# Kernel tuning notes

Hardware: AMD Instinct MI355X
Metric: run time of the kernel (lower is better)

## Reference

```python
import jax, jax.numpy as jnp
import numpy as np

UNITS = 128
ATT_UNITS = 64
NUM_HEADS = 8


def setup_inputs() -> dict:
    key = jax.random.key(0)
    ks = jax.random.split(key, 8)
    N, F, E = 50000, 128, 800000
    x = jax.random.normal(ks[0], (N, F), dtype=jnp.float32)
    edge_index = jax.random.randint(ks[1], (2, E), 0, N, dtype=jnp.int32)
    glorot = lambda k, shp: jax.random.uniform(k, shp, jnp.float32,
                                               -jnp.sqrt(6.0 / (shp[0] + shp[1])),
                                               jnp.sqrt(6.0 / (shp[0] + shp[1])))
    return {
        "x": x,
        "edge_index": edge_index,
        "query_kernel": glorot(ks[2], (F, ATT_UNITS)),
        "query_bias": jnp.zeros((ATT_UNITS,), jnp.float32),
        "key_kernel": glorot(ks[3], (F, ATT_UNITS)),
        "key_bias": jnp.zeros((ATT_UNITS,), jnp.float32),
        "kernel": glorot(ks[4], (F, UNITS)),
        "bias": jnp.zeros((UNITS,), jnp.float32),
    }


def reference(x, edge_index, query_kernel, query_bias, key_kernel, key_bias, kernel, bias):
    N = x.shape[0]
    H = NUM_HEADS
    # add self-loop edges (tf_geometric add_self_loop_edge)
    loop = jnp.arange(N, dtype=edge_index.dtype)
    row = jnp.concatenate([edge_index[0], loop])  # target nodes
    col = jnp.concatenate([edge_index[1], loop])  # source nodes
    E = row.shape[0]

    Q = jax.nn.relu(x @ query_kernel + query_bias)[row]  # [E, A]
    K = jax.nn.relu(x @ key_kernel + key_bias)[col]      # [E, A]
    V = (x @ kernel)[col]                                # [E, U]

    # split feature dim into contiguous head chunks (matches tf.split)
    Qh = Q.reshape(E, H, -1)
    Kh = K.reshape(E, H, -1)
    Vh = V.reshape(E, H, -1)

    score = jnp.sum(Qh * Kh, axis=-1)  # [E, H]
    # segment softmax over edges grouped by target node (row)
    smax = jax.ops.segment_max(score, row, num_segments=N)  # [N, H]
    ex = jnp.exp(score - smax[row])
    ssum = jax.ops.segment_sum(ex, row, num_segments=N)     # [N, H]
    alpha = ex / ssum[row]                                  # [E, H]

    agg = jax.ops.segment_sum(Vh * alpha[..., None], row, num_segments=N)  # [N, H, U/H]
    h = agg.reshape(N, -1) + bias
    return h
```

## Files before the change

### kernel.cpp

```cpp
#include <hip/hip_runtime.h>

#define SHIFT 10.0f
#define CAP 64
#define NXCD 8
#define BSH 7
#define CAPB 3072

typedef __attribute__((ext_vector_type(8))) short bf16x8;
typedef __attribute__((ext_vector_type(4))) float f32x4;
typedef _Float16 half2v __attribute__((ext_vector_type(2)));

__device__ inline uint16_t bf16r(float f) {
    uint32_t u = __float_as_uint(f);
    return (uint16_t)((u + 0x7FFFu + ((u >> 16) & 1u)) >> 16);
}
__device__ inline float bf2f(uint16_t h) {
    return __uint_as_float(((uint32_t)h) << 16);
}
__device__ inline uint32_t pack_bf16x2(float lo, float hi) {
    return (uint32_t)bf16r(lo) | ((uint32_t)bf16r(hi) << 16);
}
__device__ inline uint32_t pack_f16x2(float lo, float hi) {
    uint16_t a = __builtin_bit_cast(uint16_t, (_Float16)lo);
    uint16_t b = __builtin_bit_cast(uint16_t, (_Float16)hi);
    return (uint32_t)a | ((uint32_t)b << 16);
}
__device__ inline half2v as_h2(uint32_t u) {
    return __builtin_bit_cast(half2v, u);
}

#define ABSZ 512
#define AEPT 8
#define PREP_BLKS 32
__global__ __launch_bounds__(ABSZ) void prep_bin(
    const float* __restrict__ Wq, const float* __restrict__ Wk,
    const float* __restrict__ Wv, uint32_t* __restrict__ Wh32,
    uint32_t* __restrict__ Wl32,
    const int* __restrict__ row, const int* __restrict__ col,
    int* __restrict__ bucketCursor, uint32_t* __restrict__ inter, int E)
{
    if (blockIdx.x < PREP_BLKS) {
        int t = blockIdx.x * ABSZ + threadIdx.x;
        int c = t >> 6;
        int k2 = t & 63;
        float f0, f1;
        if (c < 64)       { f0 = Wq[(2 * k2) * 64 + c];          f1 = Wq[(2 * k2 + 1) * 64 + c]; }
        else if (c < 128) { f0 = Wk[(2 * k2) * 64 + (c - 64)];   f1 = Wk[(2 * k2 + 1) * 64 + (c - 64)]; }
        else              { f0 = Wv[(2 * k2) * 128 + (c - 128)]; f1 = Wv[(2 * k2 + 1) * 128 + (c - 128)]; }
        uint16_t h0 = bf16r(f0), h1 = bf16r(f1);
        uint16_t l0 = bf16r(f0 - bf2f(h0)), l1 = bf16r(f1 - bf2f(h1));
        Wh32[t] = (uint32_t)h0 | ((uint32_t)h1 << 16);
        Wl32[t] = (uint32_t)l0 | ((uint32_t)l1 << 16);
        return;
    }

    __shared__ int hist[512];
    __shared__ int basebuf[512];
    const int t = threadIdx.x;
    hist[t] = 0;
    __syncthreads();

    const int base0 = (blockIdx.x - PREP_BLKS) * ABSZ * AEPT;
    uint32_t pk[AEPT];
    int dg[AEPT], rk[AEPT];
#pragma unroll
    for (int k = 0; k < AEPT; ++k) {
        int e = base0 + k * ABSZ + t;
        if (e < E) {
            int r = row[e];
            int c = col[e];
            pk[k] = ((uint32_t)r << 16) | (uint32_t)c;
            dg[k] = r >> BSH;
            rk[k] = atomicAdd(&hist[dg[k]], 1);
        } else dg[k] = -1;
    }
    __syncthreads();

    {
        int h = hist[t];
        basebuf[t] = h ? atomicAdd(&bucketCursor[t], h) : 0;
    }
    __syncthreads();

#pragma unroll
    for (int k = 0; k < AEPT; ++k) {
        if (dg[k] >= 0) {
            int idx = basebuf[dg[k]] + rk[k];
            if (idx < CAPB)
                inter[(size_t)dg[k] * CAPB + idx] = pk[k];
        }
    }
}

__global__ __launch_bounds__(256) void fused_nlb(
    const uint32_t* __restrict__ inter, const int* __restrict__ bucketCursor,
    uint16_t* __restrict__ csr, int* __restrict__ deg,
    const float* __restrict__ x,
    const uint16_t* __restrict__ Wh, const uint16_t* __restrict__ Wl,
    const float* __restrict__ bq, const float* __restrict__ bk,
    uint32_t* __restrict__ Qh, uint32_t* __restrict__ Kh, uint32_t* __restrict__ Vh,
    int N, int NB)
{
    __shared__ uint16_t Ah[64][136];
    __shared__ uint16_t Al[64][136];
    __shared__ int cnt[128];

    if (blockIdx.x < NB) {
        const int b = blockIdx.x;
        const int t = threadIdx.x;
        if (t < 128) cnt[t] = 0;
        __syncthreads();

        const int count = min(bucketCursor[b], CAPB);
        const uint32_t* src = inter + (size_t)b * CAPB;
        for (int i = t; i < count; i += 256) {
            uint32_t u = src[i];
            int r = (int)(u >> 16);
            int pos = atomicAdd(&cnt[r & 127], 1);
            if (pos < CAP - 1)
                csr[(size_t)r * CAP + pos] = (uint16_t)(u & 0xFFFFu);
        }
        __syncthreads();

        const int node = (b << BSH) + t;
        if (t < 128 && node < N) deg[node] = min(cnt[t], CAP - 1);
        return;
    }

    const int tid = threadIdx.x;
    const int lane = tid & 63;
    const int wv = tid >> 6;
    const int block0 = (blockIdx.x - NB) * 64;
    if (block0 >= N) return;

    float4 v[8];
#pragma unroll
    for (int i = 0; i < 8; ++i) {
        int idx = tid + i * 256;
        int node = idx >> 5;
        int c4 = idx & 31;
        v[i] = make_float4(0.f, 0.f, 0.f, 0.f);
        if (block0 + node < N)
            v[i] = reinterpret_cast<const float4*>(x + (size_t)(block0 + node) * 128)[c4];
    }
#pragma unroll
    for (int i = 0; i < 8; ++i) {
        int idx = tid + i * 256;
        int node = idx >> 5;
        int c4 = idx & 31;
        uint16_t hx = bf16r(v[i].x), hy = bf16r(v[i].y), hz = bf16r(v[i].z), hw = bf16r(v[i].w);
        uint2 uh, ul;
        uh.x = (uint32_t)hx | ((uint32_t)hy << 16);
        uh.y = (uint32_t)hz | ((uint32_t)hw << 16);
        ul.x = (uint32_t)bf16r(v[i].x - bf2f(hx)) | ((uint32_t)bf16r(v[i].y - bf2f(hy)) << 16);
        ul.y = (uint32_t)bf16r(v[i].z - bf2f(hz)) | ((uint32_t)bf16r(v[i].w - bf2f(hw)) << 16);
        *reinterpret_cast<uint2*>(&Ah[node][c4 * 4]) = uh;
        *reinterpret_cast<uint2*>(&Al[node][c4 * 4]) = ul;
    }
    __syncthreads();

    f32x4 acc[4][4] = {};
#pragma unroll
    for (int ks = 0; ks < 4; ++ks) {
        bf16x8 bh[4], bl[4];
#pragma unroll
        for (int cf = 0; cf < 4; ++cf) {
            size_t off = (size_t)(wv * 64 + cf * 16 + (lane & 15)) * 128
                         + ks * 32 + (lane >> 4) * 8;
            bh[cf] = *reinterpret_cast<const bf16x8*>(Wh + off);
            bl[cf] = *reinterpret_cast<const bf16x8*>(Wl + off);
        }
#pragma unroll
        for (int rf = 0; rf < 4; ++rf) {
            bf16x8 ah = *reinterpret_cast<const bf16x8*>(
                &Ah[rf * 16 + (lane & 15)][ks * 32 + (lane >> 4) * 8]);
            bf16x8 al = *reinterpret_cast<const bf16x8*>(
                &Al[rf * 16 + (lane & 15)][ks * 32 + (lane >> 4) * 8]);
#pragma unroll
            for (int cf = 0; cf < 4; ++cf)
                acc[rf][cf] = __builtin_amdgcn_mfma_f32_16x16x32_bf16(
                    ah, bh[cf], acc[rf][cf], 0, 0, 0);
#pragma unroll
            for (int cf = 0; cf < 4; ++cf)
                acc[rf][cf] = __builtin_amdgcn_mfma_f32_16x16x32_bf16(
                    ah, bl[cf], acc[rf][cf], 0, 0, 0);
#pragma unroll
            for (int cf = 0; cf < 4; ++cf)
                acc[rf][cf] = __builtin_amdgcn_mfma_f32_16x16x32_bf16(
                    al, bh[cf], acc[rf][cf], 0, 0, 0);
        }
    }

#pragma unroll
    for (int rf = 0; rf < 4; ++rf) {
#pragma unroll
        for (int cf = 0; cf < 4; ++cf) {
            const int ocol = wv * 64 + cf * 16 + (lane & 15);
#pragma unroll
            for (int r = 0; r < 4; ++r) {
                const int orow = rf * 16 + (lane >> 4) * 4 + r;
                const int node = block0 + orow;
                float v2 = acc[rf][cf][r];
                if (wv == 0) {
                    v2 = fmaxf(v2 + bq[ocol], 0.f);
                    float vp = __shfl_xor(v2, 1);
                    if (node < N && !(lane & 1))
                        Qh[(size_t)node * 32 + (ocol >> 1)] = pack_f16x2(v2, vp);
                } else if (wv == 1) {
                    const int ck = ocol - 64;
                    v2 = fmaxf(v2 + bk[ck], 0.f);
                    float vp = __shfl_xor(v2, 1);
                    if (node < N && !(lane & 1))
                        Kh[(size_t)node * 32 + (ck >> 1)] = pack_f16x2(v2, vp);
                } else {
                    const int cv = ocol - 128;
                    float vp = __shfl_xor(v2, 1);
                    if (node < N && !(lane & 1))
                        Vh[(size_t)node * 64 + (cv >> 1)] = pack_bf16x2(v2, vp);
                }
            }
        }
    }
}

__global__ __launch_bounds__(256) void agg6(
    const int* __restrict__ deg_, const uint16_t* __restrict__ csr,
    const uint32_t* __restrict__ Qh, const uint32_t* __restrict__ Kh,
    const uint32_t* __restrict__ Vh, const float* __restrict__ bias,
    float* __restrict__ out, int N)
{
    __shared__ uint32_t qs[4][32];
    __shared__ float es[4][8][36];
    __shared__ int   cis[4][32];

    const int wv = threadIdx.x >> 6;
    const int lane = threadIdx.x & 63;

    const int xcd = blockIdx.x & (NXCD - 1);
    const int nslice = (N + NXCD - 1) / NXCD;
    const int ln = (blockIdx.x >> 3) * 4 + wv;
    if (ln >= nslice) return;
    const int n = xcd * nslice + ln;
    if (n >= N) return;

    const int deg = min(deg_[n], CAP - 1);
    const int tot = deg + 1;

    if (lane < 32) qs[wv][lane] = Qh[(size_t)n * 32 + lane];
    __builtin_amdgcn_wave_barrier();

    const int e2 = lane >> 1;
    const int half = lane & 1;
    const int hrow = lane >> 3;
    const float* esrow = &es[wv][hrow][0];
    const char* Kb = (const char*)Kh;
    const char* Vb = (const char*)Vh;
    const int lane4 = lane << 2;

    float accx = 0.f, accy = 0.f, accL = 0.f;

    for (int base = 0; base < tot; base += 32) {
        const int nn = min(32, tot - base);
        const int idxe = base + e2;
        const bool valide = (idxe < tot);
        int c = n;
        if (valide && idxe < deg) c = (int)csr[(size_t)n * CAP + idxe];
        if (!valide) c = 0;
        cis[wv][e2] = c << 8;

        const uint32_t koff = ((uint32_t)c << 7) + ((uint32_t)half << 6);
        const uint32_t* q16 = &qs[wv][half * 16];
#pragma unroll
        for (int hh = 0; hh < 4; ++hh) {
            uint4 kv = *reinterpret_cast<const uint4*>(Kb + koff + hh * 16);
            const uint32_t* q4 = q16 + hh * 4;
            float s = 0.f;
            s = __builtin_amdgcn_fdot2(as_h2(kv.x), as_h2(q4[0]), s, false);
            s = __builtin_amdgcn_fdot2(as_h2(kv.y), as_h2(q4[1]), s, false);
            s = __builtin_amdgcn_fdot2(as_h2(kv.z), as_h2(q4[2]), s, false);
            s = __builtin_amdgcn_fdot2(as_h2(kv.w), as_h2(q4[3]), s, false);
            es[wv][half * 4 + hh][e2] = valide ? __expf(s - SHIFT) : 0.f;
        }
        __builtin_amdgcn_wave_barrier();

        const int nn4 = (nn + 3) & ~3;
        for (int i = 0; i < nn4; i += 4) {
            int4 c4 = *reinterpret_cast<const int4*>(&cis[wv][i]);
            float4 e4 = *reinterpret_cast<const float4*>(&esrow[i]);
            uint32_t u0 = *reinterpret_cast<const uint32_t*>(Vb + (uint32_t)(c4.x + lane4));
            uint32_t u1 = *reinterpret_cast<const uint32_t*>(Vb + (uint32_t)(c4.y + lane4));
            uint32_t u2 = *reinterpret_cast<const uint32_t*>(Vb + (uint32_t)(c4.z + lane4));
            uint32_t u3 = *reinterpret_cast<const uint32_t*>(Vb + (uint32_t)(c4.w + lane4));
            accx += e4.x * __uint_as_float(u0 << 16);
            accy += e4.x * __uint_as_float(u0 & 0xFFFF0000u);
            accL += e4.x;
            accx += e4.y * __uint_as_float(u1 << 16);
            accy += e4.y * __uint_as_float(u1 & 0xFFFF0000u);
            accL += e4.y;
            accx += e4.z * __uint_as_float(u2 << 16);
            accy += e4.z * __uint_as_float(u2 & 0xFFFF0000u);
            accL += e4.z;
            accx += e4.w * __uint_as_float(u3 << 16);
            accy += e4.w * __uint_as_float(u3 & 0xFFFF0000u);
            accL += e4.w;
        }
        __builtin_amdgcn_wave_barrier();
    }

    float2 b = reinterpret_cast<const float2*>(bias)[lane];
    float inv = 1.0f / accL;
    float2 o;
    o.x = accx * inv + b.x;
    o.y = accy * inv + b.y;
    reinterpret_cast<float2*>(out)[(size_t)n * 64 + lane] = o;
}

extern "C" void kernel_launch(void* const* d_in, const int* in_sizes, int n_in,
                              void* d_out, int out_size, void* d_ws, size_t ws_size,
                              hipStream_t stream) {
    const float* x    = (const float*)d_in[0];
    const int*   ei   = (const int*)d_in[1];
    const float* Wq   = (const float*)d_in[2];
    const float* bq   = (const float*)d_in[3];
    const float* Wk   = (const float*)d_in[4];
    const float* bk   = (const float*)d_in[5];
    const float* Wv   = (const float*)d_in[6];
    const float* bias = (const float*)d_in[7];
    float* out = (float*)d_out;

    const int N = in_sizes[0] / 128;
    const int E = in_sizes[1] / 2;
    const int* row = ei;
    const int* col = ei + E;
    const int NB = (N + (1 << BSH) - 1) >> BSH;

    uint32_t* Qh     = (uint32_t*)d_ws;
    uint32_t* Kh     = Qh + (size_t)N * 32;
    uint32_t* Vh     = Kh + (size_t)N * 32;
    uint32_t* Wh32   = Vh + (size_t)N * 64;
    uint32_t* Wl32   = Wh32 + 16384;
    int*      deg    = (int*)(Wl32 + 16384);
    int*      bcur   = deg + N;
    uint32_t* inter  = (uint32_t*)(bcur + 512);
    uint16_t* csr    = (uint16_t*)(inter + (size_t)NB * CAPB);

    const int nslice = (N + NXCD - 1) / NXCD;
    const int agg_grid = ((nslice + 3) / 4) * NXCD;
    const int nl_grid = (N + 63) / 64;
    const int binA_grid = (E + ABSZ * AEPT - 1) / (ABSZ * AEPT);

    hipMemsetAsync(bcur, 0, 512 * sizeof(int), stream);
    prep_bin<<<PREP_BLKS + binA_grid, ABSZ, 0, stream>>>(
        Wq, Wk, Wv, Wh32, Wl32, row, col, bcur, inter, E);
    fused_nlb<<<NB + nl_grid, 256, 0, stream>>>(
        inter, bcur, csr, deg,
        x, (const uint16_t*)Wh32, (const uint16_t*)Wl32, bq, bk,
        Qh, Kh, Vh, N, NB);
    agg6<<<agg_grid, 256, 0, stream>>>(
        deg, csr, Qh, Kh, Vh, bias, out, N);
}
```

Before: 117.0 us.

## Restructure kernel pipeline: overlap edge binning with projection GEMM, split CSR build

Launches a small weight-prep kernel that also clears the bucket cursors, which replaces the memset. Edge binning phase A now runs in the same grid as the Q/K/V projection GEMM, and CSR finalisation moves into its own kernel. This overlaps the edge scan with the dense work. Q is now stored as fp32 and packed to f16 inside the aggregation kernel, which removes the shuffle in the GEMM epilogue but doubles Q traffic. The change adds one kernel launch, and the binning blocks now use 256 threads with 16 edges each.

```diff
diff --git a/kernel.cpp b/kernel.cpp
--- a/kernel.cpp
+++ b/kernel.cpp
@@ -29,108 +29,85 @@
     return __builtin_bit_cast(half2v, u);
 }
 
-#define ABSZ 512
-#define AEPT 8
-#define PREP_BLKS 32
-__global__ __launch_bounds__(ABSZ) void prep_bin(
+__global__ __launch_bounds__(256) void prep_w(
     const float* __restrict__ Wq, const float* __restrict__ Wk,
     const float* __restrict__ Wv, uint32_t* __restrict__ Wh32,
-    uint32_t* __restrict__ Wl32,
+    uint32_t* __restrict__ Wl32, int* __restrict__ bucketCursor)
+{
+    int t = blockIdx.x * 256 + threadIdx.x;
+    if (t < 512) bucketCursor[t] = 0;
+    if (t >= 256 * 64) return;
+    int c = t >> 6;
+    int k2 = t & 63;
+    float f0, f1;
+    if (c < 64)       { f0 = Wq[(2 * k2) * 64 + c];          f1 = Wq[(2 * k2 + 1) * 64 + c]; }
+    else if (c < 128) { f0 = Wk[(2 * k2) * 64 + (c - 64)];   f1 = Wk[(2 * k2 + 1) * 64 + (c - 64)]; }
+    else              { f0 = Wv[(2 * k2) * 128 + (c - 128)]; f1 = Wv[(2 * k2 + 1) * 128 + (c - 128)]; }
+    uint16_t h0 = bf16r(f0), h1 = bf16r(f1);
+    uint16_t l0 = bf16r(f0 - bf2f(h0)), l1 = bf16r(f1 - bf2f(h1));
+    Wh32[t] = (uint32_t)h0 | ((uint32_t)h1 << 16);
+    Wl32[t] = (uint32_t)l0 | ((uint32_t)l1 << 16);
+}
+
+#define AEPT 16
+__global__ __launch_bounds__(256) void nl_bin(
     const int* __restrict__ row, const int* __restrict__ col,
-    int* __restrict__ bucketCursor, uint32_t* __restrict__ inter, int E)
-{
-    if (blockIdx.x < PREP_BLKS) {
-        int t = blockIdx.x * ABSZ + threadIdx.x;
-        int c = t >> 6;
-        int k2 = t & 63;
-        float f0, f1;
-        if (c < 64)       { f0 = Wq[(2 * k2) * 64 + c];          f1 = Wq[(2 * k2 + 1) * 64 + c]; }
-        else if (c < 128) { f0 = Wk[(2 * k2) * 64 + (c - 64)];   f1 = Wk[(2 * k2 + 1) * 64 + (c - 64)]; }
-        else              { f0 = Wv[(2 * k2) * 128 + (c - 128)]; f1 = Wv[(2 * k2 + 1) * 128 + (c - 128)]; }
-        uint16_t h0 = bf16r(f0), h1 = bf16r(f1);
-        uint16_t l0 = bf16r(f0 - bf2f(h0)), l1 = bf16r(f1 - bf2f(h1));
-        Wh32[t] = (uint32_t)h0 | ((uint32_t)h1 << 16);
-        Wl32[t] = (uint32_t)l0 | ((uint32_t)l1 << 16);
-        return;
-    }
-
-    __shared__ int hist[512];
-    __shared__ int basebuf[512];
-    const int t = threadIdx.x;
-    hist[t] = 0;
-    __syncthreads();
-
-    const int base0 = (blockIdx.x - PREP_BLKS) * ABSZ * AEPT;
-    uint32_t pk[AEPT];
-    int dg[AEPT], rk[AEPT];
-#pragma unroll
-    for (int k = 0; k < AEPT; ++k) {
-        int e = base0 + k * ABSZ + t;
-        if (e < E) {
-            int r = row[e];
-            int c = col[e];
-            pk[k] = ((uint32_t)r << 16) | (uint32_t)c;
-            dg[k] = r >> BSH;
-            rk[k] = atomicAdd(&hist[dg[k]], 1);
-        } else dg[k] = -1;
-    }
-    __syncthreads();
-
-    {
-        int h = hist[t];
-        basebuf[t] = h ? atomicAdd(&bucketCursor[t], h) : 0;
-    }
-    __syncthreads();
-
-#pragma unroll
-    for (int k = 0; k < AEPT; ++k) {
-        if (dg[k] >= 0) {
-            int idx = basebuf[dg[k]] + rk[k];
-            if (idx < CAPB)
-                inter[(size_t)dg[k] * CAPB + idx] = pk[k];
-        }
-    }
-}
-
-__global__ __launch_bounds__(256) void fused_nlb(
-    const uint32_t* __restrict__ inter, const int* __restrict__ bucketCursor,
-    uint16_t* __restrict__ csr, int* __restrict__ deg,
+    int* __restrict__ bucketCursor, uint32_t* __restrict__ inter, int E,
     const float* __restrict__ x,
     const uint16_t* __restrict__ Wh, const uint16_t* __restrict__ Wl,
     const float* __restrict__ bq, const float* __restrict__ bk,
-    uint32_t* __restrict__ Qh, uint32_t* __restrict__ Kh, uint32_t* __restrict__ Vh,
-    int N, int NB)
+    float* __restrict__ Qn, uint32_t* __restrict__ Kh, uint32_t* __restrict__ Vh,
+    int N, int NLG)
 {
     __shared__ uint16_t Ah[64][136];
     __shared__ uint16_t Al[64][136];
-    __shared__ int cnt[128];
-
-    if (blockIdx.x < NB) {
-        const int b = blockIdx.x;
+    __shared__ int hist[512];
+    __shared__ int basebuf[512];
+
+    if (blockIdx.x >= NLG) {
         const int t = threadIdx.x;
-        if (t < 128) cnt[t] = 0;
+        hist[t] = 0; hist[t + 256] = 0;
         __syncthreads();
 
-        const int count = min(bucketCursor[b], CAPB);
-        const uint32_t* src = inter + (size_t)b * CAPB;
-        for (int i = t; i < count; i += 256) {
-            uint32_t u = src[i];
-            int r = (int)(u >> 16);
-            int pos = atomicAdd(&cnt[r & 127], 1);
-            if (pos < CAP - 1)
-                csr[(size_t)r * CAP + pos] = (uint16_t)(u & 0xFFFFu);
+        const int base0 = (blockIdx.x - NLG) * 256 * AEPT;
+        uint32_t pk[AEPT];
+        int dg[AEPT], rk[AEPT];
+#pragma unroll
+        for (int k = 0; k < AEPT; ++k) {
+            int e = base0 + k * 256 + t;
+            if (e < E) {
+                int r = row[e];
+                int c = col[e];
+                pk[k] = ((uint32_t)r << 16) | (uint32_t)c;
+                dg[k] = r >> BSH;
+                rk[k] = atomicAdd(&hist[dg[k]], 1);
+            } else dg[k] = -1;
         }
         __syncthreads();
 
-        const int node = (b << BSH) + t;
-        if (t < 128 && node < N) deg[node] = min(cnt[t], CAP - 1);
+#pragma unroll
+        for (int b2 = 0; b2 < 2; ++b2) {
+            int i = t + b2 * 256;
+            int h = hist[i];
+            basebuf[i] = h ? atomicAdd(&bucketCursor[i], h) : 0;
+        }
+        __syncthreads();
+
+#pragma unroll
+        for (int k = 0; k < AEPT; ++k) {
+            if (dg[k] >= 0) {
+                int idx = basebuf[dg[k]] + rk[k];
+                if (idx < CAPB)
+                    inter[(size_t)dg[k] * CAPB + idx] = pk[k];
+            }
+        }
         return;
     }
 
     const int tid = threadIdx.x;
     const int lane = tid & 63;
     const int wv = tid >> 6;
-    const int block0 = (blockIdx.x - NB) * 64;
+    const int block0 = blockIdx.x * 64;
     if (block0 >= N) return;
 
     float4 v[8];
@@ -203,9 +180,7 @@
                 float v2 = acc[rf][cf][r];
                 if (wv == 0) {
                     v2 = fmaxf(v2 + bq[ocol], 0.f);
-                    float vp = __shfl_xor(v2, 1);
-                    if (node < N && !(lane & 1))
-                        Qh[(size_t)node * 32 + (ocol >> 1)] = pack_f16x2(v2, vp);
+                    if (node < N) Qn[(size_t)node * 64 + ocol] = v2;
                 } else if (wv == 1) {
                     const int ck = ocol - 64;
                     v2 = fmaxf(v2 + bk[ck], 0.f);
@@ -223,9 +198,34 @@
     }
 }
 
+__global__ __launch_bounds__(256) void bin_b(
+    const uint32_t* __restrict__ inter, const int* __restrict__ bucketCursor,
+    uint16_t* __restrict__ csr, int* __restrict__ deg, int N)
+{
+    __shared__ int cnt[128];
+    const int b = blockIdx.x;
+    const int t = threadIdx.x;
+    if (t < 128) cnt[t] = 0;
+    __syncthreads();
+
+    const int count = min(bucketCursor[b], CAPB);
+    const uint32_t* src = inter + (size_t)b * CAPB;
+    for (int i = t; i < count; i += 256) {
+        uint32_t u = src[i];
+        int r = (int)(u >> 16);
+        int pos = atomicAdd(&cnt[r & 127], 1);
+        if (pos < CAP - 1)
+            csr[(size_t)r * CAP + pos] = (uint16_t)(u & 0xFFFFu);
+    }
+    __syncthreads();
+
+    const int node = (b << BSH) + t;
+    if (t < 128 && node < N) deg[node] = min(cnt[t], CAP - 1);
+}
+
 __global__ __launch_bounds__(256) void agg6(
     const int* __restrict__ deg_, const uint16_t* __restrict__ csr,
-    const uint32_t* __restrict__ Qh, const uint32_t* __restrict__ Kh,
+    const float* __restrict__ Qn, const uint32_t* __restrict__ Kh,
     const uint32_t* __restrict__ Vh, const float* __restrict__ bias,
     float* __restrict__ out, int N)
 {
@@ -246,7 +246,10 @@
     const int deg = min(deg_[n], CAP - 1);
     const int tot = deg + 1;
 
-    if (lane < 32) qs[wv][lane] = Qh[(size_t)n * 32 + lane];
+    if (lane < 32) {
+        float2 qq = reinterpret_cast<const float2*>(Qn + (size_t)n * 64)[lane];
+        qs[wv][lane] = pack_f16x2(qq.x, qq.y);
+    }
     __builtin_amdgcn_wave_barrier();
 
     const int e2 = lane >> 1;
@@ -334,8 +337,8 @@
     const int* col = ei + E;
     const int NB = (N + (1 << BSH) - 1) >> BSH;
 
-    uint32_t* Qh     = (uint32_t*)d_ws;
-    uint32_t* Kh     = Qh + (size_t)N * 32;
+    float*    Qn     = (float*)d_ws;
+    uint32_t* Kh     = (uint32_t*)(Qn + (size_t)N * 64);
     uint32_t* Vh     = Kh + (size_t)N * 32;
     uint32_t* Wh32   = Vh + (size_t)N * 64;
     uint32_t* Wl32   = Wh32 + 16384;
@@ -347,15 +350,14 @@
     const int nslice = (N + NXCD - 1) / NXCD;
     const int agg_grid = ((nslice + 3) / 4) * NXCD;
     const int nl_grid = (N + 63) / 64;
-    const int binA_grid = (E + ABSZ * AEPT - 1) / (ABSZ * AEPT);
-
-    hipMemsetAsync(bcur, 0, 512 * sizeof(int), stream);
-    prep_bin<<<PREP_BLKS + binA_grid, ABSZ, 0, stream>>>(
-        Wq, Wk, Wv, Wh32, Wl32, row, col, bcur, inter, E);
-    fused_nlb<<<NB + nl_grid, 256, 0, stream>>>(
-        inter, bcur, csr, deg,
+    const int binA_grid = (E + 256 * AEPT - 1) / (256 * AEPT);
+
+    prep_w<<<64, 256, 0, stream>>>(Wq, Wk, Wv, Wh32, Wl32, bcur);
+    nl_bin<<<nl_grid + binA_grid, 256, 0, stream>>>(
+        row, col, bcur, inter, E,
         x, (const uint16_t*)Wh32, (const uint16_t*)Wl32, bq, bk,
-        Qh, Kh, Vh, N, NB);
+        Qn, Kh, Vh, N, nl_grid);
+    bin_b<<<NB, 256, 0, stream>>>(inter, bcur, csr, deg, N);
     agg6<<<agg_grid, 256, 0, stream>>>(
-        deg, csr, Qh, Kh, Vh, bias, out, N);
-}
+        deg, csr, Qn, Kh, Vh, bias, out, N);
+}
```

Result: faster. 109.3 us (-6.5%).

## Use persistent grid-stride tiles for projection GEMM and store Q as fp32

Applied to the files above, without the earlier changes.

The node projection part of fused_nlb now runs on a fixed 512-block grid that loops over 64-node tiles, instead of launching one block per tile. This amortizes block launch cost and may keep the weight fragments warm across tiles. The Q output is now written as unpacked fp32 without the shuffle, and agg6 packs it to fp16 when it loads it. That removes the shuffle from the GEMM epilogue but doubles the bytes of Q written and then read back.

```diff
diff --git a/kernel.cpp b/kernel.cpp
--- a/kernel.cpp
+++ b/kernel.cpp
@@ -5,6 +5,7 @@
 #define NXCD 8
 #define BSH 7
 #define CAPB 3072
+#define NL_BLKS 512
 
 typedef __attribute__((ext_vector_type(8))) short bf16x8;
 typedef __attribute__((ext_vector_type(4))) float f32x4;
@@ -98,7 +99,7 @@
     const float* __restrict__ x,
     const uint16_t* __restrict__ Wh, const uint16_t* __restrict__ Wl,
     const float* __restrict__ bq, const float* __restrict__ bk,
-    uint32_t* __restrict__ Qh, uint32_t* __restrict__ Kh, uint32_t* __restrict__ Vh,
+    float* __restrict__ Qn, uint32_t* __restrict__ Kh, uint32_t* __restrict__ Vh,
     int N, int NB)
 {
     __shared__ uint16_t Ah[64][136];
@@ -130,102 +131,104 @@
     const int tid = threadIdx.x;
     const int lane = tid & 63;
     const int wv = tid >> 6;
-    const int block0 = (blockIdx.x - NB) * 64;
-    if (block0 >= N) return;
-
-    float4 v[8];
-#pragma unroll
-    for (int i = 0; i < 8; ++i) {
-        int idx = tid + i * 256;
-        int node = idx >> 5;
-        int c4 = idx & 31;
-        v[i] = make_float4(0.f, 0.f, 0.f, 0.f);
-        if (block0 + node < N)
-            v[i] = reinterpret_cast<const float4*>(x + (size_t)(block0 + node) * 128)[c4];
-    }
-#pragma unroll
-    for (int i = 0; i < 8; ++i) {
-        int idx = tid + i * 256;
-        int node = idx >> 5;
-        int c4 = idx & 31;
-        uint16_t hx = bf16r(v[i].x), hy = bf16r(v[i].y), hz = bf16r(v[i].z), hw = bf16r(v[i].w);
-        uint2 uh, ul;
-        uh.x = (uint32_t)hx | ((uint32_t)hy << 16);
-        uh.y = (uint32_t)hz | ((uint32_t)hw << 16);
-        ul.x = (uint32_t)bf16r(v[i].x - bf2f(hx)) | ((uint32_t)bf16r(v[i].y - bf2f(hy)) << 16);
-        ul.y = (uint32_t)bf16r(v[i].z - bf2f(hz)) | ((uint32_t)bf16r(v[i].w - bf2f(hw)) << 16);
-        *reinterpret_cast<uint2*>(&Ah[node][c4 * 4]) = uh;
-        *reinterpret_cast<uint2*>(&Al[node][c4 * 4]) = ul;
-    }
-    __syncthreads();
-
-    f32x4 acc[4][4] = {};
-#pragma unroll
-    for (int ks = 0; ks < 4; ++ks) {
-        bf16x8 bh[4], bl[4];
-#pragma unroll
-        for (int cf = 0; cf < 4; ++cf) {
-            size_t off = (size_t)(wv * 64 + cf * 16 + (lane & 15)) * 128
-                         + ks * 32 + (lane >> 4) * 8;
-            bh[cf] = *reinterpret_cast<const bf16x8*>(Wh + off);
-            bl[cf] = *reinterpret_cast<const bf16x8*>(Wl + off);
-        }
+    const int ntiles = (N + 63) >> 6;
+
+    for (int tile = blockIdx.x - NB; tile < ntiles; tile += NL_BLKS) {
+        const int block0 = tile * 64;
+
+        float4 v[8];
+#pragma unroll
+        for (int i = 0; i < 8; ++i) {
+            int idx = tid + i * 256;
+            int node = idx >> 5;
+            int c4 = idx & 31;
+            v[i] = make_float4(0.f, 0.f, 0.f, 0.f);
+            if (block0 + node < N)
+                v[i] = reinterpret_cast<const float4*>(x + (size_t)(block0 + node) * 128)[c4];
+        }
+#pragma unroll
+        for (int i = 0; i < 8; ++i) {
+            int idx = tid + i * 256;
+            int node = idx >> 5;
+            int c4 = idx & 31;
+            uint16_t hx = bf16r(v[i].x), hy = bf16r(v[i].y), hz = bf16r(v[i].z), hw = bf16r(v[i].w);
+            uint2 uh, ul;
+            uh.x = (uint32_t)hx | ((uint32_t)hy << 16);
+            uh.y = (uint32_t)hz | ((uint32_t)hw << 16);
+            ul.x = (uint32_t)bf16r(v[i].x - bf2f(hx)) | ((uint32_t)bf16r(v[i].y - bf2f(hy)) << 16);
+            ul.y = (uint32_t)bf16r(v[i].z - bf2f(hz)) | ((uint32_t)bf16r(v[i].w - bf2f(hw)) << 16);
+            *reinterpret_cast<uint2*>(&Ah[node][c4 * 4]) = uh;
+            *reinterpret_cast<uint2*>(&Al[node][c4 * 4]) = ul;
+        }
+        __syncthreads();
+
+        f32x4 acc[4][4] = {};
+#pragma unroll
+        for (int ks = 0; ks < 4; ++ks) {
+            bf16x8 bh[4], bl[4];
+#pragma unroll
+            for (int cf = 0; cf < 4; ++cf) {
+                size_t off = (size_t)(wv * 64 + cf * 16 + (lane & 15)) * 128
+                             + ks * 32 + (lane >> 4) * 8;
+                bh[cf] = *reinterpret_cast<const bf16x8*>(Wh + off);
+                bl[cf] = *reinterpret_cast<const bf16x8*>(Wl + off);
+            }
+#pragma unroll
+            for (int rf = 0; rf < 4; ++rf) {
+                bf16x8 ah = *reinterpret_cast<const bf16x8*>(
+                    &Ah[rf * 16 + (lane & 15)][ks * 32 + (lane >> 4) * 8]);
+                bf16x8 al = *reinterpret_cast<const bf16x8*>(
+                    &Al[rf * 16 + (lane & 15)][ks * 32 + (lane >> 4) * 8]);
+#pragma unroll
+                for (int cf = 0; cf < 4; ++cf)
+                    acc[rf][cf] = __builtin_amdgcn_mfma_f32_16x16x32_bf16(
+                        ah, bh[cf], acc[rf][cf], 0, 0, 0);
+#pragma unroll
+                for (int cf = 0; cf < 4; ++cf)
+                    acc[rf][cf] = __builtin_amdgcn_mfma_f32_16x16x32_bf16(
+                        ah, bl[cf], acc[rf][cf], 0, 0, 0);
+#pragma unroll
+                for (int cf = 0; cf < 4; ++cf)
+                    acc[rf][cf] = __builtin_amdgcn_mfma_f32_16x16x32_bf16(
+                        al, bh[cf], acc[rf][cf], 0, 0, 0);
+            }
+        }
+
 #pragma unroll
         for (int rf = 0; rf < 4; ++rf) {
-            bf16x8 ah = *reinterpret_cast<const bf16x8*>(
-                &Ah[rf * 16 + (lane & 15)][ks * 32 + (lane >> 4) * 8]);
-            bf16x8 al = *reinterpret_cast<const bf16x8*>(
-                &Al[rf * 16 + (lane & 15)][ks * 32 + (lane >> 4) * 8]);
-#pragma unroll
-            for (int cf = 0; cf < 4; ++cf)
-                acc[rf][cf] = __builtin_amdgcn_mfma_f32_16x16x32_bf16(
-                    ah, bh[cf], acc[rf][cf], 0, 0, 0);
-#pragma unroll
-            for (int cf = 0; cf < 4; ++cf)
-                acc[rf][cf] = __builtin_amdgcn_mfma_f32_16x16x32_bf16(
-                    ah, bl[cf], acc[rf][cf], 0, 0, 0);
-#pragma unroll
-            for (int cf = 0; cf < 4; ++cf)
-                acc[rf][cf] = __builtin_amdgcn_mfma_f32_16x16x32_bf16(
-                    al, bh[cf], acc[rf][cf], 0, 0, 0);
-        }
-    }
-
-#pragma unroll
-    for (int rf = 0; rf < 4; ++rf) {
-#pragma unroll
-        for (int cf = 0; cf < 4; ++cf) {
-            const int ocol = wv * 64 + cf * 16 + (lane & 15);
-#pragma unroll
-            for (int r = 0; r < 4; ++r) {
-                const int orow = rf * 16 + (lane >> 4) * 4 + r;
-                const int node = block0 + orow;
-                float v2 = acc[rf][cf][r];
-                if (wv == 0) {
-                    v2 = fmaxf(v2 + bq[ocol], 0.f);
-                    float vp = __shfl_xor(v2, 1);
-                    if (node < N && !(lane & 1))
-                        Qh[(size_t)node * 32 + (ocol >> 1)] = pack_f16x2(v2, vp);
-                } else if (wv == 1) {
-                    const int ck = ocol - 64;
-                    v2 = fmaxf(v2 + bk[ck], 0.f);
-                    float vp = __shfl_xor(v2, 1);
-                    if (node < N && !(lane & 1))
-                        Kh[(size_t)node * 32 + (ck >> 1)] = pack_f16x2(v2, vp);
-                } else {
-                    const int cv = ocol - 128;
-                    float vp = __shfl_xor(v2, 1);
-                    if (node < N && !(lane & 1))
-                        Vh[(size_t)node * 64 + (cv >> 1)] = pack_bf16x2(v2, vp);
+#pragma unroll
+            for (int cf = 0; cf < 4; ++cf) {
+                const int ocol = wv * 64 + cf * 16 + (lane & 15);
+#pragma unroll
+                for (int r = 0; r < 4; ++r) {
+                    const int orow = rf * 16 + (lane >> 4) * 4 + r;
+                    const int node = block0 + orow;
+                    float v2 = acc[rf][cf][r];
+                    if (wv == 0) {
+                        v2 = fmaxf(v2 + bq[ocol], 0.f);
+                        if (node < N) Qn[(size_t)node * 64 + ocol] = v2;
+                    } else if (wv == 1) {
+                        const int ck = ocol - 64;
+                        v2 = fmaxf(v2 + bk[ck], 0.f);
+                        float vp = __shfl_xor(v2, 1);
+                        if (node < N && !(lane & 1))
+                            Kh[(size_t)node * 32 + (ck >> 1)] = pack_f16x2(v2, vp);
+                    } else {
+                        const int cv = ocol - 128;
+                        float vp = __shfl_xor(v2, 1);
+                        if (node < N && !(lane & 1))
+                            Vh[(size_t)node * 64 + (cv >> 1)] = pack_bf16x2(v2, vp);
+                    }
                 }
             }
         }
+        __syncthreads();
     }
 }
 
 __global__ __launch_bounds__(256) void agg6(
     const int* __restrict__ deg_, const uint16_t* __restrict__ csr,
-    const uint32_t* __restrict__ Qh, const uint32_t* __restrict__ Kh,
+    const float* __restrict__ Qn, const uint32_t* __restrict__ Kh,
     const uint32_t* __restrict__ Vh, const float* __restrict__ bias,
     float* __restrict__ out, int N)
 {
@@ -246,7 +249,10 @@
     const int deg = min(deg_[n], CAP - 1);
     const int tot = deg + 1;
 
-    if (lane < 32) qs[wv][lane] = Qh[(size_t)n * 32 + lane];
+    if (lane < 32) {
+        float2 qq = reinterpret_cast<const float2*>(Qn + (size_t)n * 64)[lane];
+        qs[wv][lane] = pack_f16x2(qq.x, qq.y);
+    }
     __builtin_amdgcn_wave_barrier();
 
     const int e2 = lane >> 1;
@@ -334,8 +340,8 @@
     const int* col = ei + E;
     const int NB = (N + (1 << BSH) - 1) >> BSH;
 
-    uint32_t* Qh     = (uint32_t*)d_ws;
-    uint32_t* Kh     = Qh + (size_t)N * 32;
+    float*    Qn     = (float*)d_ws;
+    uint32_t* Kh     = (uint32_t*)(Qn + (size_t)N * 64);
     uint32_t* Vh     = Kh + (size_t)N * 32;
     uint32_t* Wh32   = Vh + (size_t)N * 64;
     uint32_t* Wl32   = Wh32 + 16384;
@@ -346,16 +352,15 @@
 
     const int nslice = (N + NXCD - 1) / NXCD;
     const int agg_grid = ((nslice + 3) / 4) * NXCD;
-    const int nl_grid = (N + 63) / 64;
     const int binA_grid = (E + ABSZ * AEPT - 1) / (ABSZ * AEPT);
 
     hipMemsetAsync(bcur, 0, 512 * sizeof(int), stream);
     prep_bin<<<PREP_BLKS + binA_grid, ABSZ, 0, stream>>>(
         Wq, Wk, Wv, Wh32, Wl32, row, col, bcur, inter, E);
-    fused_nlb<<<NB + nl_grid, 256, 0, stream>>>(
+    fused_nlb<<<NB + NL_BLKS, 256, 0, stream>>>(
         inter, bcur, csr, deg,
         x, (const uint16_t*)Wh32, (const uint16_t*)Wl32, bq, bk,
-        Qh, Kh, Vh, N, NB);
+        Qn, Kh, Vh, N, NB);
     agg6<<<agg_grid, 256, 0, stream>>>(
-        deg, csr, Qh, Kh, Vh, bias, out, N);
-}
+        deg, csr, Qn, Kh, Vh, bias, out, N);
+}
```

Measured after the change: 143.5 us. 22.7% more time.
